# Kernel optimization log

Hardware: AMD Instinct MI355X
Metric: run time of the kernel (lower is better)

Reference implementation:

```python
import jax, jax.numpy as jnp
import numpy as np
import math

D_MODEL = 1024
N_HEADS = 16
HEAD_DIM = D_MODEL // N_HEADS
PAD_INDEX = 0
NEG_INF = -1e9  # matches torch masked_fill value


def setup_inputs() -> dict:
    key = jax.random.key(0)
    ks = jax.random.split(key, 10)
    b, s = 2, 2048
    x = jax.random.normal(ks[0], (b, s, D_MODEL), dtype=jnp.float32)
    input_ids = jax.random.randint(ks[1], (b, s), 0, 32000, dtype=jnp.int64)
    scale = 1.0 / math.sqrt(D_MODEL)
    def lin(k):
        kw, kb = jax.random.split(k)
        W = jax.random.uniform(kw, (D_MODEL, D_MODEL), jnp.float32, -scale, scale)
        bb = jax.random.uniform(kb, (D_MODEL,), jnp.float32, -scale, scale)
        return W, bb
    Wq, bq = lin(ks[2])
    Wk, bk = lin(ks[3])
    Wv, bv = lin(ks[4])
    Wo, bo = lin(ks[5])
    return {"x": x, "input_ids": input_ids,
            "Wq": Wq, "bq": bq, "Wk": Wk, "bk": bk,
            "Wv": Wv, "bv": bv, "Wo": Wo, "bo": bo}


def reference(x, input_ids, Wq, bq, Wk, bk, Wv, bv, Wo, bo):
    b, s, _ = x.shape
    # torch nn.Linear: y = x @ W.T + b
    q = (x @ Wq.T + bq).reshape(b, s, N_HEADS, HEAD_DIM)
    k = (x @ Wk.T + bk).reshape(b, s, N_HEADS, HEAD_DIM)
    v = (x @ Wv.T + bv).reshape(b, s, N_HEADS, HEAD_DIM)
    # scores: [b, h, s, s]
    scores = jnp.einsum('bqhd,bkhd->bhqk', q, k) / math.sqrt(HEAD_DIM)
    pad_mask = (input_ids != PAD_INDEX)[:, None, None, :]          # [b,1,1,s] over keys
    causal = jnp.tril(jnp.ones((s, s), dtype=bool))[None, None]     # [1,1,s,s]
    final_mask = pad_mask & causal
    scores = jnp.where(final_mask, scores, NEG_INF)
    attn = jax.nn.softmax(scores, axis=-1)
    out = jnp.einsum('bhqk,bkhd->bqhd', attn, v).reshape(b, s, D_MODEL)
    return out @ Wo.T + bo
```

## Files before the change

### kernel.cpp

```cpp
#include <hip/hip_runtime.h>

#define DMODEL 1024
#define NHEADS 16
#define HDIM   64
#define BATCH  2
#define SEQ    2048
#define MROWS  (BATCH*SEQ)

typedef __bf16 bf16x8 __attribute__((ext_vector_type(8)));
typedef __bf16 bf16x4 __attribute__((ext_vector_type(4)));
typedef float floatx4 __attribute__((ext_vector_type(4)));

typedef const __attribute__((address_space(1))) void gvoid;
typedef __attribute__((address_space(3))) void lvoid;

template<bool V> struct ICb { static constexpr bool value = V; };

#define QSCALE 0.18033688011112042f

__global__ void cast_all(const float* __restrict__ x,
                         const float* __restrict__ wq, const float* __restrict__ wk,
                         const float* __restrict__ wv, const float* __restrict__ wo,
                         __bf16* __restrict__ xb, __bf16* __restrict__ wqb,
                         __bf16* __restrict__ wkb, __bf16* __restrict__ wvb,
                         __bf16* __restrict__ wob)
{
  const int i = blockIdx.x * 256 + threadIdx.x;
  const float* s; __bf16* o; int off;
  if (i < MROWS*DMODEL/4) { s = x; o = xb; off = i; }
  else {
    const int r = i - MROWS*DMODEL/4;
    const int w = r >> 18;
    off = r & 262143;
    s = (w == 0) ? wq : (w == 1) ? wk : (w == 2) ? wv : wo;
    o = (w == 0) ? wqb : (w == 1) ? wkb : (w == 2) ? wvb : wob;
  }
  const float4 f = ((const float4*)s)[off];
  bf16x4 v = {(__bf16)f.x, (__bf16)f.y, (__bf16)f.z, (__bf16)f.w};
  *(bf16x4*)(o + off*4) = v;
}

template<int MODE>
__global__ __launch_bounds__(256, 3)
void gemm_nt(const unsigned short* __restrict__ A,
             const unsigned short* __restrict__ W0,
             const unsigned short* __restrict__ W1,
             const unsigned short* __restrict__ W2,
             const float* __restrict__ b0,
             const float* __restrict__ b1,
             const float* __restrict__ b2,
             unsigned short* __restrict__ qout,
             unsigned short* __restrict__ kout,
             unsigned short* __restrict__ vout,
             float* __restrict__ outf)
{
  const int K = DMODEL;
  __shared__ unsigned short As[2][128*32];
  __shared__ unsigned short Bs[2][128*32];
  const int tid  = threadIdx.x;
  const int wid  = tid >> 6;
  const int lane = tid & 63;

  const int lin = blockIdx.x;
  const int wg  = (MODE == 0) ? ((lin & 7)*96 + (lin >> 3))
                              : ((lin & 7)*32 + (lin >> 3));
  const int bx  = (MODE == 0) ? (wg % 24) : (wg & 7);
  const int by  = (MODE == 0) ? (wg / 24) : (wg >> 3);
  const int brow = by * 128;
  const int bcol = bx * 128;
  const int wr = (wid >> 1) * 64;
  const int wc = (wid & 1) * 64;

  int which = 0;
  const unsigned short* Bw = W0;
  const float* bias = b0;
  int bcolL = bcol;
  if (MODE == 0) {
    which = bcol >> 10;
    Bw   = which == 0 ? W0 : which == 1 ? W1 : W2;
    bias = which == 0 ? b0 : which == 1 ? b1 : b2;
    bcolL = bcol & 1023;
  }

  floatx4 acc[4][4] = {};

  const int sr = wid*16 + (lane >> 2);
  const int sc = (lane & 3) * 8;
  const int fr = lane & 15;
  const int fk = (lane >> 4) * 8;

#define GSTAGE(KT, B) do {                                                     \
    _Pragma("unroll")                                                          \
    for (int i_ = 0; i_ < 2; ++i_) {                                           \
      __builtin_amdgcn_global_load_lds(                                        \
          (gvoid*)(A + (size_t)(brow + i_*64 + sr)*K + (KT) + sc),             \
          (lvoid*)(As[B] + i_*2048 + wid*512), 16, 0, 0);                      \
      __builtin_amdgcn_global_load_lds(                                        \
          (gvoid*)(Bw + (size_t)(bcolL + i_*64 + sr)*K + (KT) + sc),           \
          (lvoid*)(Bs[B] + i_*2048 + wid*512), 16, 0, 0);                      \
    }                                                                          \
  } while (0)

  GSTAGE(0, 0);

  for (int kt = 0; kt < K; kt += 32) {
    const int cur = (kt >> 5) & 1;
    if (kt + 32 < K) {
      GSTAGE(kt + 32, cur ^ 1);
      asm volatile("s_waitcnt vmcnt(4)" ::: "memory");
    } else {
      asm volatile("s_waitcnt vmcnt(0)" ::: "memory");
    }
    __builtin_amdgcn_s_barrier();
    __builtin_amdgcn_sched_barrier(0);

    bf16x8 af[4], bfv[4];
#pragma unroll
    for (int m = 0; m < 4; ++m)
      af[m] = *(const bf16x8*)(As[cur] + (wr + m*16 + fr)*32 + fk);
#pragma unroll
    for (int n = 0; n < 4; ++n)
      bfv[n] = *(const bf16x8*)(Bs[cur] + (wc + n*16 + fr)*32 + fk);
    __builtin_amdgcn_s_setprio(1);
#pragma unroll
    for (int m = 0; m < 4; ++m)
#pragma unroll
      for (int n = 0; n < 4; ++n)
        acc[m][n] = __builtin_amdgcn_mfma_f32_16x16x32_bf16(af[m], bfv[n], acc[m][n], 0, 0, 0);
    __builtin_amdgcn_s_setprio(0);
    __builtin_amdgcn_s_barrier();
  }
#undef GSTAGE

  const int er = (lane >> 4) * 4;
  const int ec = lane & 15;
#pragma unroll
  for (int m = 0; m < 4; ++m) {
#pragma unroll
    for (int n = 0; n < 4; ++n) {
      const int colL = bcolL + wc + n*16 + ec;
      const float bv = bias[colL];
      const int rowb = brow + wr + m*16 + er;
      if (MODE == 0) {
        const int bi = rowb >> 11, s = rowb & 2047;
        const int hh = colL >> 6, dd = colL & 63;
        if (which == 2) {
          bf16x4 v4 = {(__bf16)(acc[m][n][0] + bv), (__bf16)(acc[m][n][1] + bv),
                       (__bf16)(acc[m][n][2] + bv), (__bf16)(acc[m][n][3] + bv)};
          *(bf16x4*)((__bf16*)vout + ((size_t)(bi*NHEADS + hh)*HDIM + dd)*SEQ + s) = v4;
        } else if (which == 0) {
          __bf16* o = (__bf16*)qout;
#pragma unroll
          for (int j = 0; j < 4; ++j)
            o[((size_t)(bi*NHEADS + hh)*SEQ + s + j)*HDIM + dd] =
                (__bf16)((acc[m][n][j] + bv) * QSCALE);
        } else {
          __bf16* o = (__bf16*)kout;
#pragma unroll
          for (int j = 0; j < 4; ++j)
            o[((size_t)(bi*NHEADS + hh)*SEQ + s + j)*HDIM + dd] = (__bf16)(acc[m][n][j] + bv);
        }
      } else {
#pragma unroll
        for (int j = 0; j < 4; ++j)
          outf[(size_t)(rowb + j)*DMODEL + colL] = acc[m][n][j] + bv;
      }
    }
  }
}

__global__ __launch_bounds__(512, 4)
void attn_fwd(const unsigned short* __restrict__ qb,
              const unsigned short* __restrict__ kb,
              const unsigned short* __restrict__ vtb,
              const int* __restrict__ ids,
              unsigned short* __restrict__ outb)
{
  const int bx = blockIdx.x;
  const int hb = bx & 31;
  const int qt = 31 - (bx >> 5);
  const int h = hb & 15, bi = hb >> 4;

  const int tid = threadIdx.x, wid = tid >> 6, lane = tid & 63;
  const int grp  = wid >> 2;
  const int wid4 = wid & 3;
  const int qbase = qt * 64;
  const size_t hoff = (size_t)(bi*NHEADS + h) * SEQ * HDIM;
  const unsigned short* Qh  = qb  + hoff;
  const unsigned short* Kh  = kb  + hoff;
  const unsigned short* Vth = vtb + hoff;

  __shared__ unsigned short Ks[2][2][64*64];
  __shared__ unsigned short Vs[2][2][64*64];
  __shared__ unsigned short Ps[8][16*64];
  float* LOf = (float*)Ps;
  float* Ll  = (float*)Ks;

  const int q_   = lane & 15;
  const int hi4  = lane >> 4;
  const int koff = hi4 * 4;
  const int qg = qbase + wid4*16 + q_;

  bf16x8 qf[2];
#pragma unroll
  for (int c = 0; c < 2; ++c)
    qf[c] = *(const bf16x8*)(Qh + (size_t)qg*HDIM + c*32 + hi4*8);

  const int gt = tid & 255;
  const int r0 = gt >> 3;
  const int sw = ((gt & 7) ^ (r0 & 7)) * 8;
  unsigned short* Pw = Ps[wid];

#define STAGE(T, B) do {                                                       \
    const unsigned short* kbase_ = Kh + (size_t)((T)*64) * HDIM;               \
    const unsigned short* vbase_ = Vth + (T)*64;                               \
    __builtin_amdgcn_global_load_lds((gvoid*)(kbase_ + r0*64 + sw),            \
                                     (lvoid*)(Ks[grp][B] + gt*8), 16, 0, 0);   \
    __builtin_amdgcn_global_load_lds((gvoid*)(kbase_ + (r0+32)*64 + sw),       \
                                     (lvoid*)(Ks[grp][B] + (gt+256)*8), 16, 0, 0);\
    __builtin_amdgcn_global_load_lds((gvoid*)(vbase_ + (size_t)r0*SEQ + sw),   \
                                     (lvoid*)(Vs[grp][B] + gt*8), 16, 0, 0);   \
    __builtin_amdgcn_global_load_lds((gvoid*)(vbase_ + (size_t)(r0+32)*SEQ + sw),\
                                     (lvoid*)(Vs[grp][B] + (gt+256)*8), 16, 0, 0);\
  } while (0)

  float lsum = 0.f;
  floatx4 Oacc[4] = {};

  auto step = [&](auto Mc, int kb0, int bufc, unsigned long long wm) {
    constexpr bool MASKED = decltype(Mc)::value;

    floatx4 st[4];
    __builtin_amdgcn_s_setprio(1);
#pragma unroll
    for (int t = 0; t < 4; ++t) {
      st[t] = (floatx4){0.f, 0.f, 0.f, 0.f};
      const int kr = t*16 + q_;
#pragma unroll
      for (int c = 0; c < 2; ++c) {
        const int cd = ((c*4 + hi4) ^ (kr & 7)) * 8;
        bf16x8 kf = *(const bf16x8*)(Ks[grp][bufc] + kr*64 + cd);
        st[t] = __builtin_amdgcn_mfma_f32_16x16x32_bf16(kf, qf[c], st[t], 0, 0, 0);
      }
    }
    __builtin_amdgcn_s_setprio(0);

    float ps = 0.f;
#pragma unroll
    for (int t = 0; t < 4; ++t) {
      float p[4];
#pragma unroll
      for (int r = 0; r < 4; ++r) {
        float pv = exp2f(st[t][r]);
        if (MASKED) {
          const int ko = t*16 + koff + r;
          const bool dead = ((kb0 + ko) > qg) || (((wm >> ko) & 1ull) != 0ull);
          pv = dead ? 0.f : pv;
        }
        p[r] = pv;
        ps += pv;
      }
      bf16x4 pk = {(__bf16)p[0], (__bf16)p[1], (__bf16)p[2], (__bf16)p[3]};
      const int ko = t*16 + koff;
      *(bf16x4*)(Pw + q_*64 + (((ko >> 3) ^ (q_ & 7)) * 8) + (ko & 7)) = pk;
    }
    lsum += ps;

    __builtin_amdgcn_s_setprio(1);
#pragma unroll
    for (int cp = 0; cp < 2; ++cp) {
      const int ko = cp*32 + hi4*8;
      bf16x8 pf = *(const bf16x8*)(Pw + q_*64 + (((ko >> 3) ^ (q_ & 7)) * 8));
#pragma unroll
      for (int n = 0; n < 4; ++n) {
        const int d = n*16 + q_;
        const int cd = ((cp*4 + hi4) ^ (d & 7)) * 8;
        bf16x8 vf = *(const bf16x8*)(Vs[grp][bufc] + d*64 + cd);
        Oacc[n] = __builtin_amdgcn_mfma_f32_16x16x32_bf16(pf, vf, Oacc[n], 0, 0, 0);
      }
    }
    __builtin_amdgcn_s_setprio(0);
  };

  const int nT = qt + 1;
  const int h0 = (nT + 1) >> 1;
  const int cnt = (grp == 0) ? h0 : nT - h0;
  const int tb  = (grp == 0) ? 0 : h0;
  const int H = h0;

  if (cnt > 0) STAGE(tb, 0);

  for (int i = 0; i < H; ++i) {
    const bool valid = (i < cnt);
    const int t = tb + i;
    const int kb0 = t * 64;
    int pv = 1;
    if (valid) pv = ids[bi*SEQ + kb0 + lane];
    if (i + 1 < cnt) {
      STAGE(t + 1, (i + 1) & 1);
      asm volatile("s_waitcnt vmcnt(4)" ::: "memory");
    } else {
      asm volatile("s_waitcnt vmcnt(0)" ::: "memory");
    }
    const unsigned long long wm = __ballot(pv == 0);
    __builtin_amdgcn_s_barrier();
    __builtin_amdgcn_sched_barrier(0);

    if (valid) {
      const int bufc = i & 1;
      if ((t != nT - 1) && wm == 0ull) step(ICb<false>{}, kb0, bufc, 0ull);
      else                             step(ICb<true >{}, kb0, bufc, wm);
    }
    __builtin_amdgcn_s_barrier();
  }
#undef STAGE

  float lt = lsum + __shfl_xor(lsum, 16);
  lt += __shfl_xor(lt, 32);

  if (grp == 1) {
#pragma unroll
    for (int r = 0; r < 4; ++r)
#pragma unroll
      for (int n = 0; n < 4; ++n)
        LOf[(wid4*16 + koff + r)*64 + n*16 + q_] = Oacc[n][r];
    if (hi4 == 0) Ll[wid4*16 + q_] = lt;
  }
  __syncthreads();
  if (grp == 0) {
#pragma unroll
    for (int r = 0; r < 4; ++r) {
      const int rloc = wid4*16 + koff + r;
      const float inv = 1.f / (__shfl(lt, koff + r) + Ll[rloc]);
      const int row = bi*SEQ + qbase + rloc;
#pragma unroll
      for (int n = 0; n < 4; ++n) {
        const float o = Oacc[n][r] + LOf[rloc*64 + n*16 + q_];
        ((__bf16*)outb)[(size_t)row*DMODEL + h*HDIM + n*16 + q_] = (__bf16)(o * inv);
      }
    }
  }
}

extern "C" void kernel_launch(void* const* d_in, const int* in_sizes, int n_in,
                              void* d_out, int out_size, void* d_ws, size_t ws_size,
                              hipStream_t stream)
{
  const float* x  = (const float*)d_in[0];
  const int*   ids= (const int*)d_in[1];
  const float* Wq = (const float*)d_in[2];
  const float* bq = (const float*)d_in[3];
  const float* Wk = (const float*)d_in[4];
  const float* bk = (const float*)d_in[5];
  const float* Wv = (const float*)d_in[6];
  const float* bv = (const float*)d_in[7];
  const float* Wo = (const float*)d_in[8];
  const float* bo = (const float*)d_in[9];
  float* out = (float*)d_out;

  char* ws = (char*)d_ws;
  unsigned short* xb   = (unsigned short*)(ws);
  unsigned short* wqb  = (unsigned short*)(ws + ( 8u<<20));
  unsigned short* wkb  = (unsigned short*)(ws + (10u<<20));
  unsigned short* wvb  = (unsigned short*)(ws + (12u<<20));
  unsigned short* wob  = (unsigned short*)(ws + (14u<<20));
  unsigned short* qbuf = (unsigned short*)(ws + (16u<<20));
  unsigned short* kbuf = (unsigned short*)(ws + (24u<<20));
  unsigned short* vbuf = (unsigned short*)(ws + (32u<<20));
  unsigned short* abuf = (unsigned short*)(ws + (40u<<20));

  cast_all<<<8192, 256, 0, stream>>>(x, Wq, Wk, Wv, Wo,
                                     (__bf16*)xb, (__bf16*)wqb, (__bf16*)wkb,
                                     (__bf16*)wvb, (__bf16*)wob);

  gemm_nt<0><<<768, 256, 0, stream>>>(xb, wqb, wkb, wvb, bq, bk, bv,
                                      qbuf, kbuf, vbuf, nullptr);

  attn_fwd<<<1024, 512, 0, stream>>>(qbuf, kbuf, vbuf, ids, abuf);

  gemm_nt<1><<<256, 256, 0, stream>>>(abuf, wob, wob, wob, bo, bo, bo,
                                      nullptr, nullptr, nullptr, out);
}
```

Before: 111.6 us.

## Drop double buffering in attention to shrink LDS and double occupancy

The attention kernel stops double-buffering K/V tiles and drops the separate P buffer. P now lives in the K buffer after a barrier, and the output reduction reuses V's space. That cuts LDS per block by roughly a factor of three, and launch bounds move to 8 blocks per CU to raise occupancy. The grid becomes 2D with a serpentine ordering of query tiles, aiming at better load balance across the causal triangle. In exchange, each iteration now waits synchronously on its loads with an extra barrier, so global load latency is no longer overlapped within a block and must be hidden by the other resident blocks.

```diff
diff --git a/kernel.cpp b/kernel.cpp
--- a/kernel.cpp
+++ b/kernel.cpp
@@ -13,8 +13,6 @@
 
 typedef const __attribute__((address_space(1))) void gvoid;
 typedef __attribute__((address_space(3))) void lvoid;
-
-template<bool V> struct ICb { static constexpr bool value = V; };
 
 #define QSCALE 0.18033688011112042f
 
@@ -169,17 +167,18 @@
   }
 }
 
-__global__ __launch_bounds__(512, 4)
+__global__ __launch_bounds__(512, 8)
 void attn_fwd(const unsigned short* __restrict__ qb,
               const unsigned short* __restrict__ kb,
               const unsigned short* __restrict__ vtb,
               const int* __restrict__ ids,
               unsigned short* __restrict__ outb)
 {
-  const int bx = blockIdx.x;
-  const int hb = bx & 31;
-  const int qt = 31 - (bx >> 5);
+  const int hb = blockIdx.x;
   const int h = hb & 15, bi = hb >> 4;
+  const int y = blockIdx.y;
+  const int jm = y >> 3, mm = y & 7;
+  const int qt = jm*8 + ((jm & 1) ? 7 - mm : mm);
 
   const int tid = threadIdx.x, wid = tid >> 6, lane = tid & 63;
   const int grp  = wid >> 2;
@@ -190,10 +189,9 @@
   const unsigned short* Kh  = kb  + hoff;
   const unsigned short* Vth = vtb + hoff;
 
-  __shared__ unsigned short Ks[2][2][64*64];
-  __shared__ unsigned short Vs[2][2][64*64];
-  __shared__ unsigned short Ps[8][16*64];
-  float* LOf = (float*)Ps;
+  __shared__ unsigned short Ks[2][64*64];
+  __shared__ unsigned short Vs[2][64*64];
+  float* LOf = (float*)Vs;
   float* Ll  = (float*)Ks;
 
   const int q_   = lane & 15;
@@ -209,109 +207,101 @@
   const int gt = tid & 255;
   const int r0 = gt >> 3;
   const int sw = ((gt & 7) ^ (r0 & 7)) * 8;
-  unsigned short* Pw = Ps[wid];
-
-#define STAGE(T, B) do {                                                       \
+  unsigned short* Pw = Ks[grp] + wid4*1024;
+
+#define STAGE(T) do {                                                          \
     const unsigned short* kbase_ = Kh + (size_t)((T)*64) * HDIM;               \
     const unsigned short* vbase_ = Vth + (T)*64;                               \
     __builtin_amdgcn_global_load_lds((gvoid*)(kbase_ + r0*64 + sw),            \
-                                     (lvoid*)(Ks[grp][B] + gt*8), 16, 0, 0);   \
+                                     (lvoid*)(Ks[grp] + gt*8), 16, 0, 0);      \
     __builtin_amdgcn_global_load_lds((gvoid*)(kbase_ + (r0+32)*64 + sw),       \
-                                     (lvoid*)(Ks[grp][B] + (gt+256)*8), 16, 0, 0);\
+                                     (lvoid*)(Ks[grp] + (gt+256)*8), 16, 0, 0);\
     __builtin_amdgcn_global_load_lds((gvoid*)(vbase_ + (size_t)r0*SEQ + sw),   \
-                                     (lvoid*)(Vs[grp][B] + gt*8), 16, 0, 0);   \
+                                     (lvoid*)(Vs[grp] + gt*8), 16, 0, 0);      \
     __builtin_amdgcn_global_load_lds((gvoid*)(vbase_ + (size_t)(r0+32)*SEQ + sw),\
-                                     (lvoid*)(Vs[grp][B] + (gt+256)*8), 16, 0, 0);\
+                                     (lvoid*)(Vs[grp] + (gt+256)*8), 16, 0, 0);\
   } while (0)
 
   float lsum = 0.f;
   floatx4 Oacc[4] = {};
-
-  auto step = [&](auto Mc, int kb0, int bufc, unsigned long long wm) {
-    constexpr bool MASKED = decltype(Mc)::value;
-
-    floatx4 st[4];
-    __builtin_amdgcn_s_setprio(1);
-#pragma unroll
-    for (int t = 0; t < 4; ++t) {
-      st[t] = (floatx4){0.f, 0.f, 0.f, 0.f};
-      const int kr = t*16 + q_;
-#pragma unroll
-      for (int c = 0; c < 2; ++c) {
-        const int cd = ((c*4 + hi4) ^ (kr & 7)) * 8;
-        bf16x8 kf = *(const bf16x8*)(Ks[grp][bufc] + kr*64 + cd);
-        st[t] = __builtin_amdgcn_mfma_f32_16x16x32_bf16(kf, qf[c], st[t], 0, 0, 0);
-      }
-    }
-    __builtin_amdgcn_s_setprio(0);
-
-    float ps = 0.f;
-#pragma unroll
-    for (int t = 0; t < 4; ++t) {
-      float p[4];
-#pragma unroll
-      for (int r = 0; r < 4; ++r) {
-        float pv = exp2f(st[t][r]);
-        if (MASKED) {
-          const int ko = t*16 + koff + r;
-          const bool dead = ((kb0 + ko) > qg) || (((wm >> ko) & 1ull) != 0ull);
-          pv = dead ? 0.f : pv;
-        }
-        p[r] = pv;
-        ps += pv;
-      }
-      bf16x4 pk = {(__bf16)p[0], (__bf16)p[1], (__bf16)p[2], (__bf16)p[3]};
-      const int ko = t*16 + koff;
-      *(bf16x4*)(Pw + q_*64 + (((ko >> 3) ^ (q_ & 7)) * 8) + (ko & 7)) = pk;
-    }
-    lsum += ps;
-
-    __builtin_amdgcn_s_setprio(1);
-#pragma unroll
-    for (int cp = 0; cp < 2; ++cp) {
-      const int ko = cp*32 + hi4*8;
-      bf16x8 pf = *(const bf16x8*)(Pw + q_*64 + (((ko >> 3) ^ (q_ & 7)) * 8));
-#pragma unroll
-      for (int n = 0; n < 4; ++n) {
-        const int d = n*16 + q_;
-        const int cd = ((cp*4 + hi4) ^ (d & 7)) * 8;
-        bf16x8 vf = *(const bf16x8*)(Vs[grp][bufc] + d*64 + cd);
-        Oacc[n] = __builtin_amdgcn_mfma_f32_16x16x32_bf16(pf, vf, Oacc[n], 0, 0, 0);
-      }
-    }
-    __builtin_amdgcn_s_setprio(0);
-  };
 
   const int nT = qt + 1;
   const int h0 = (nT + 1) >> 1;
   const int cnt = (grp == 0) ? h0 : nT - h0;
   const int tb  = (grp == 0) ? 0 : h0;
-  const int H = h0;
-
-  if (cnt > 0) STAGE(tb, 0);
-
-  for (int i = 0; i < H; ++i) {
+
+  for (int i = 0; i < h0; ++i) {
     const bool valid = (i < cnt);
     const int t = tb + i;
     const int kb0 = t * 64;
-    int pv = 1;
-    if (valid) pv = ids[bi*SEQ + kb0 + lane];
-    if (i + 1 < cnt) {
-      STAGE(t + 1, (i + 1) & 1);
-      asm volatile("s_waitcnt vmcnt(4)" ::: "memory");
-    } else {
-      asm volatile("s_waitcnt vmcnt(0)" ::: "memory");
-    }
-    const unsigned long long wm = __ballot(pv == 0);
+    int pvv = 1;
+    if (valid) {
+      pvv = ids[bi*SEQ + kb0 + lane];
+      STAGE(t);
+    }
+    asm volatile("s_waitcnt vmcnt(0)" ::: "memory");
+    const unsigned long long wm = __ballot(pvv == 0);
     __builtin_amdgcn_s_barrier();
     __builtin_amdgcn_sched_barrier(0);
 
+    floatx4 st[4];
     if (valid) {
-      const int bufc = i & 1;
-      if ((t != nT - 1) && wm == 0ull) step(ICb<false>{}, kb0, bufc, 0ull);
-      else                             step(ICb<true >{}, kb0, bufc, wm);
-    }
-    __builtin_amdgcn_s_barrier();
+#pragma unroll
+      for (int t2 = 0; t2 < 4; ++t2) {
+        st[t2] = (floatx4){0.f, 0.f, 0.f, 0.f};
+        const int kr = t2*16 + q_;
+#pragma unroll
+        for (int c = 0; c < 2; ++c) {
+          const int cd = ((c*4 + hi4) ^ (kr & 7)) * 8;
+          bf16x8 kf = *(const bf16x8*)(Ks[grp] + kr*64 + cd);
+          st[t2] = __builtin_amdgcn_mfma_f32_16x16x32_bf16(kf, qf[c], st[t2], 0, 0, 0);
+        }
+      }
+    }
+    __syncthreads();
+
+    if (valid) {
+      const bool maskstep = (t == nT - 1) || (wm != 0ull);
+      float p[16];
+      if (!maskstep) {
+#pragma unroll
+        for (int j = 0; j < 16; ++j) p[j] = exp2f(st[j >> 2][j & 3]);
+      } else {
+#pragma unroll
+        for (int t2 = 0; t2 < 4; ++t2)
+#pragma unroll
+          for (int r = 0; r < 4; ++r) {
+            const int ko = t2*16 + koff + r;
+            const bool dead = ((kb0 + ko) > qg) || (((wm >> ko) & 1ull) != 0ull);
+            p[t2*4+r] = dead ? 0.f : exp2f(st[t2][r]);
+          }
+      }
+      float ps = 0.f;
+#pragma unroll
+      for (int t2 = 0; t2 < 4; ++t2) {
+        ps += ((p[t2*4] + p[t2*4+1]) + (p[t2*4+2] + p[t2*4+3]));
+        bf16x4 pk = {(__bf16)p[t2*4], (__bf16)p[t2*4+1], (__bf16)p[t2*4+2], (__bf16)p[t2*4+3]};
+        const int ko = t2*16 + koff;
+        *(bf16x4*)(Pw + q_*64 + (((ko >> 3) ^ (q_ & 7)) * 8) + (ko & 7)) = pk;
+      }
+      lsum += ps;
+
+      __builtin_amdgcn_s_setprio(1);
+#pragma unroll
+      for (int cp = 0; cp < 2; ++cp) {
+        const int ko = cp*32 + hi4*8;
+        bf16x8 pf = *(const bf16x8*)(Pw + q_*64 + (((ko >> 3) ^ (q_ & 7)) * 8));
+#pragma unroll
+        for (int n = 0; n < 4; ++n) {
+          const int d = n*16 + q_;
+          const int cd = ((cp*4 + hi4) ^ (d & 7)) * 8;
+          bf16x8 vf = *(const bf16x8*)(Vs[grp] + d*64 + cd);
+          Oacc[n] = __builtin_amdgcn_mfma_f32_16x16x32_bf16(pf, vf, Oacc[n], 0, 0, 0);
+        }
+      }
+      __builtin_amdgcn_s_setprio(0);
+    }
+    __syncthreads();
   }
 #undef STAGE
 
@@ -376,7 +366,7 @@
   gemm_nt<0><<<768, 256, 0, stream>>>(xb, wqb, wkb, wvb, bq, bk, bv,
                                       qbuf, kbuf, vbuf, nullptr);
 
-  attn_fwd<<<1024, 512, 0, stream>>>(qbuf, kbuf, vbuf, ids, abuf);
+  attn_fwd<<<dim3(32, 32), 512, 0, stream>>>(qbuf, kbuf, vbuf, ids, abuf);
 
   gemm_nt<1><<<256, 256, 0, stream>>>(abuf, wob, wob, wob, bo, bo, bo,
                                       nullptr, nullptr, nullptr, out);
```

After: 236.7 us. +112.0%, slower.
